# Optimization experiments

Hardware: AMD Instinct MI355X
Metric: run time of the kernel (lower is better)

## Reference

```python
import jax, jax.numpy as jnp
import numpy as np

B, N, C, H = 32, 384, 768, 12
EPS = 1e-6

def setup_inputs() -> dict:
    key = jax.random.key(0)
    k0, k1, k2, k3 = jax.random.split(key, 4)
    x = jax.random.normal(k0, (B, N, C), dtype=jnp.float32)
    # binary keep-mask over key tokens, broadcastable to [B,1,N,N]
    policy = (jax.random.uniform(k1, (B, 1, 1, N)) > 0.5).astype(jnp.float32)
    qkv_w = jax.random.normal(k2, (3 * C, C), dtype=jnp.float32) * 0.02
    qkv_b = jnp.zeros((3 * C,), dtype=jnp.float32)
    proj_w = jax.random.normal(k3, (C, C), dtype=jnp.float32) * 0.02
    proj_b = jnp.zeros((C,), dtype=jnp.float32)
    return {"x": x, "policy": policy, "qkv_w": qkv_w, "qkv_b": qkv_b,
            "proj_w": proj_w, "proj_b": proj_b}

def reference(x, policy, qkv_w, qkv_b, proj_w, proj_b):
    b, n, c = x.shape
    hd = c // H
    scale = hd ** -0.5
    qkv = (x @ qkv_w.T + qkv_b).reshape(b, n, 3, H, hd).transpose(2, 0, 3, 1, 4)
    q, k, v = qkv[0], qkv[1], qkv[2]
    attn = jnp.einsum('bhnd,bhmd->bhnm', q, k) * scale  # [B,H,N,N]
    # softmax_with_policy: eye-blend so every token attends to itself,
    # then eps-regularized masked softmax
    eye = jnp.eye(n, dtype=policy.dtype)[None, None]  # [1,1,N,N]
    attn_policy = policy + (1.0 - policy) * eye       # broadcast -> [B,1,N,N]
    max_att = attn.max(axis=-1, keepdims=True)
    e = jnp.exp(attn - max_att) * attn_policy
    attn = (e + EPS / n) / (e.sum(axis=-1, keepdims=True) + EPS)
    out = jnp.einsum('bhnm,bhmd->bnhd', attn, v).reshape(b, n, c)
    return out @ proj_w.T + proj_b
```

## Files before the change

### kernel.cpp

```cpp
#include <hip/hip_runtime.h>

#define BB 32
#define NN 384
#define CC 768
#define HH 12
#define HD 64

typedef __attribute__((ext_vector_type(4))) float f32x4;
typedef __attribute__((ext_vector_type(8))) __bf16 bf16x8;
typedef __attribute__((ext_vector_type(4))) __bf16 bf16x4;

static __device__ __forceinline__ f32x4 mfma16(bf16x8 a, bf16x8 b, f32x4 c) {
    return __builtin_amdgcn_mfma_f32_16x16x32_bf16(a, b, c, 0, 0, 0);
}

static __device__ __forceinline__ void gload_lds16(const void* g, void* l) {
    __builtin_amdgcn_global_load_lds((const __attribute__((address_space(1))) void*)g,
                                     (__attribute__((address_space(3))) void*)l, 16, 0, 0);
}

#define XU   1179648
#define QU   73728
#define QKVU 221184
#define PU   73728
__global__ void cvt_kernel(const float* __restrict__ x, const float* __restrict__ qkv_w,
                           const float* __restrict__ proj_w, __bf16* __restrict__ dst) {
    const int i = blockIdx.x * blockDim.x + threadIdx.x;
    if (i >= XU + QKVU + PU) return;
    const float* src;
    float sc = 1.f;
    if (i < XU) src = x + (size_t)i * 8;
    else if (i < XU + QKVU) {
        src = qkv_w + (size_t)(i - XU) * 8;
        if (i < XU + QU) sc = 0.125f;
    } else src = proj_w + (size_t)(i - XU - QKVU) * 8;
    f32x4 a = *(const f32x4*)src;
    f32x4 b = *(const f32x4*)(src + 4);
    bf16x8 o;
#pragma unroll
    for (int j = 0; j < 4; ++j) { o[j] = (__bf16)(a[j] * sc); o[j + 4] = (__bf16)(b[j] * sc); }
    *(bf16x8*)(dst + (size_t)i * 8) = o;
}

template <int EPI>
__global__ __launch_bounds__(256, 2) void gemm_kernel(
    const __bf16* __restrict__ A, const __bf16* __restrict__ Bw,
    const float* __restrict__ bias,
    __bf16* __restrict__ qkbuf, __bf16* __restrict__ vtbuf,
    float* __restrict__ fout) {
    __shared__ __bf16 SA[2][128 * 64];
    __shared__ __bf16 SB[2][128 * 64];

    const int tid = threadIdx.x;
    const int l = tid & 63;
    const int w = tid >> 6;
    const int g = l >> 4, q16 = l & 15;
    const int mb = blockIdx.x * 128;
    const int nb = blockIdx.y * 128;
    const int wrb = (w >> 1) * 64;
    const int wcb = (w & 1) * 64;
    const int swz = q16 & 7;

    auto stage = [&](int buf, int kt) {
#pragma unroll
        for (int j = 0; j < 4; ++j) {
            const int ci = j * 256 + w * 64 + l;
            const int row = ci >> 3, c = ci & 7;
            const size_t go = (size_t)row * CC + kt * 64 + ((c ^ (row & 7)) << 3);
            gload_lds16(&A[(size_t)mb * CC + go], &SA[buf][(j * 256 + w * 64) * 8]);
            gload_lds16(&Bw[(size_t)nb * CC + go], &SB[buf][(j * 256 + w * 64) * 8]);
        }
    };

    f32x4 acc[4][4] = {};

    stage(0, 0);
    __syncthreads();

    for (int kt = 0; kt < 12; ++kt) {
        const int buf = kt & 1;
        if (kt < 11) stage(buf ^ 1, kt + 1);
        const char* pa = (const char*)&SA[buf][0];
        const char* pb = (const char*)&SB[buf][0];
#pragma unroll
        for (int c4 = 0; c4 < 2; ++c4) {
            bf16x8 af[4], bfr[4];
#pragma unroll
            for (int m = 0; m < 4; ++m)
                af[m] = *(const bf16x8*)(pa + (wrb + m * 16 + q16) * 128 +
                                         (((c4 * 4 + g) ^ swz) << 4));
#pragma unroll
            for (int n = 0; n < 4; ++n)
                bfr[n] = *(const bf16x8*)(pb + (wcb + n * 16 + q16) * 128 +
                                          (((c4 * 4 + g) ^ swz) << 4));
            __builtin_amdgcn_s_setprio(1);
#pragma unroll
            for (int m = 0; m < 4; ++m)
#pragma unroll
                for (int n = 0; n < 4; ++n)
                    acc[m][n] = mfma16(af[m], bfr[n], acc[m][n]);
            __builtin_amdgcn_s_setprio(0);
        }
        __syncthreads();
    }

    if constexpr (EPI == 0) {
        const int bbatch = mb / NN;
        const int tokb = mb % NN;
#pragma unroll
        for (int n = 0; n < 4; ++n) {
            const int colb = nb + wcb + n * 16;
            const int col = colb + q16;
            float bs = bias[col];
            if (colb < 2 * CC) {
                if (colb < CC) bs *= 0.125f;
#pragma unroll
                for (int m = 0; m < 4; ++m) {
                    const int row = mb + wrb + m * 16 + g * 4;
#pragma unroll
                    for (int r = 0; r < 4; ++r)
                        qkbuf[(size_t)(row + r) * 1536 + col] = (__bf16)(acc[m][n][r] + bs);
                }
            } else {
                const int dd = (col - 2 * CC) & 63;
                const int hh = (colb - 2 * CC) >> 6;
                __bf16* vp = vtbuf + ((size_t)(bbatch * HH + hh) * HD + dd) * NN;
#pragma unroll
                for (int m = 0; m < 4; ++m) {
                    const int tok = tokb + wrb + m * 16 + g * 4;
                    bf16x4 pk;
#pragma unroll
                    for (int r = 0; r < 4; ++r) pk[r] = (__bf16)(acc[m][n][r] + bs);
                    *(bf16x4*)&vp[tok] = pk;
                }
            }
        }
    } else {
#pragma unroll
        for (int n = 0; n < 4; ++n) {
            const int col = nb + wcb + n * 16 + q16;
            const float bs = bias[col];
#pragma unroll
            for (int m = 0; m < 4; ++m)
#pragma unroll
                for (int r = 0; r < 4; ++r)
                    fout[(size_t)(mb + wrb + m * 16 + g * 4 + r) * CC + col] = acc[m][n][r] + bs;
        }
    }
}

__global__ __launch_bounds__(512, 1) void attn_kernel(
    const __bf16* __restrict__ qkbuf, const __bf16* __restrict__ vtbuf,
    const float* __restrict__ policy, __bf16* __restrict__ attb) {
    __shared__ __bf16 Qlds[NN * HD];
    __shared__ __bf16 Klds[NN * HD];
    __shared__ __bf16 Vlds[HD * NN];
    __shared__ float pol[NN];

    const int tid = threadIdx.x;
    const int l = tid & 63;
    const int w = tid >> 6;
    const int g = l >> 4, q16 = l & 15;
    const int bh = blockIdx.x;
    const int b = bh / HH, h = bh % HH;

    const __bf16* qg = qkbuf + (size_t)b * NN * 1536 + h * HD;
    const __bf16* kg = qg + CC;
#pragma unroll
    for (int p = 0; p < 6; ++p) {
        const int cs = p * 512 + w * 64 + l;
        const int row = cs >> 3, cin = cs & 7;
        const size_t go = (size_t)row * 1536 + (size_t)((cin ^ (row & 7)) << 3);
        gload_lds16(&qg[go], &Qlds[(p * 512 + w * 64) * 8]);
        gload_lds16(&kg[go], &Klds[(p * 512 + w * 64) * 8]);
    }
    const __bf16* vg = vtbuf + (size_t)(b * HH + h) * HD * NN;
#pragma unroll
    for (int p = 0; p < 6; ++p) {
        const int cs = p * 512 + w * 64 + l;
        const int row = cs / 48, cin = cs - row * 48;
        gload_lds16(&vg[row * NN + ((cin ^ (row & 7)) << 3)], &Vlds[(p * 512 + w * 64) * 8]);
    }
    for (int i = tid; i < NN; i += 512) pol[i] = policy[b * NN + i];
    __syncthreads();

    const int sw = (q16 & 7) << 4;

    unsigned kw0 = 0, kw1 = 0, kw2 = 0;
#pragma unroll
    for (int kt = 0; kt < 6; ++kt)
#pragma unroll
        for (int t = 0; t < 4; ++t)
#pragma unroll
            for (int r = 0; r < 4; ++r) {
                const int key = kt * 64 + t * 16 + g * 4 + r;
                const unsigned bset = (pol[key] > 0.5f) ? 1u : 0u;
                const int bit = kt * 16 + t * 4 + r;
                if (bit < 32) kw0 |= bset << bit;
                else if (bit < 64) kw1 |= bset << (bit - 32);
                else kw2 |= bset << (bit - 64);
            }

#pragma unroll 1
    for (int ps = 0; ps < 3; ++ps) {
        const int qrow = ps * 128 + w * 16 + q16;
        const int qbyte0 = qrow * 128 + g * 16;
        const bf16x8 qf0 = *(const bf16x8*)((const char*)Qlds + (qbyte0 ^ sw));
        const bf16x8 qf1 = *(const bf16x8*)((const char*)Qlds + ((qbyte0 + 64) ^ sw));

        unsigned pw0 = kw0, pw1 = kw1, pw2 = kw2;
        if (((qrow >> 2) & 3) == g) {
            const int sbit = (qrow >> 6) * 16 + ((qrow >> 4) & 3) * 4 + (qrow & 3);
            if (sbit < 32) pw0 |= 1u << sbit;
            else if (sbit < 64) pw1 |= 1u << (sbit - 32);
            else pw2 |= 1u << (sbit - 64);
        }

        f32x4 oacc[4] = {};
        f32x4 ssum = {0.f, 0.f, 0.f, 0.f};

#pragma unroll 2
        for (int kt = 0; kt < 6; ++kt) {
            f32x4 st[4];
            __builtin_amdgcn_s_setprio(1);
#pragma unroll
            for (int t = 0; t < 4; ++t) {
                const int byte0 = ((kt * 4 + t) * 16 + q16) * 128 + g * 16;
                bf16x8 k0 = *(const bf16x8*)((const char*)Klds + (byte0 ^ sw));
                bf16x8 k1 = *(const bf16x8*)((const char*)Klds + ((byte0 + 64) ^ sw));
                f32x4 z = {0.f, 0.f, 0.f, 0.f};
                st[t] = mfma16(k1, qf1, mfma16(k0, qf0, z));
            }
            __builtin_amdgcn_s_setprio(0);

#pragma unroll
            for (int t = 0; t < 4; ++t) {
#pragma unroll
                for (int r = 0; r < 4; ++r) {
                    const int bit = kt * 16 + t * 4 + r;
                    const unsigned wsel = (bit < 32) ? pw0 : ((bit < 64) ? pw1 : pw2);
                    const bool keep = (wsel >> (bit & 31)) & 1u;
                    st[t][r] = keep ? __expf(st[t][r]) : 0.f;
                }
                ssum += st[t];
            }

            __builtin_amdgcn_s_setprio(1);
#pragma unroll
            for (int c4 = 0; c4 < 2; ++c4) {
                bf16x8 pf;
#pragma unroll
                for (int r = 0; r < 4; ++r) {
                    pf[r] = (__bf16)st[2 * c4][r];
                    pf[r + 4] = (__bf16)st[2 * c4 + 1][r];
                }
                const int c = kt * 2 + c4;
#pragma unroll
                for (int db = 0; db < 4; ++db) {
                    const int byte0 = (db * 16 + q16) * 768 + c * 64 + g * 8;
                    bf16x4 v0 = *(const bf16x4*)((const char*)Vlds + (byte0 ^ sw));
                    bf16x4 v1 = *(const bf16x4*)((const char*)Vlds + ((byte0 + 32) ^ sw));
                    bf16x8 vf;
#pragma unroll
                    for (int r = 0; r < 4; ++r) { vf[r] = v0[r]; vf[r + 4] = v1[r]; }
                    oacc[db] = mfma16(vf, pf, oacc[db]);
                }
            }
            __builtin_amdgcn_s_setprio(0);
        }

        float sum = (ssum[0] + ssum[1]) + (ssum[2] + ssum[3]);
        sum += __shfl_xor(sum, 16);
        sum += __shfl_xor(sum, 32);
        const float dinv = 1.f / (sum + 1e-6f);

        __bf16* op = attb + ((size_t)b * NN + qrow) * CC + h * HD;
#pragma unroll
        for (int db = 0; db < 4; ++db) {
            bf16x4 pk;
#pragma unroll
            for (int r = 0; r < 4; ++r) pk[r] = (__bf16)(oacc[db][r] * dinv);
            *(bf16x4*)&op[db * 16 + g * 4] = pk;
        }
    }
}

extern "C" void kernel_launch(void* const* d_in, const int* in_sizes, int n_in,
                              void* d_out, int out_size, void* d_ws, size_t ws_size,
                              hipStream_t stream) {
    (void)in_sizes; (void)n_in; (void)out_size; (void)ws_size;
    const float* x      = (const float*)d_in[0];
    const float* policy = (const float*)d_in[1];
    const float* qkv_w  = (const float*)d_in[2];
    const float* qkv_b  = (const float*)d_in[3];
    const float* proj_w = (const float*)d_in[4];
    const float* proj_b = (const float*)d_in[5];
    float* out = (float*)d_out;

    __bf16* xb    = (__bf16*)d_ws;
    __bf16* wqkv  = xb + (size_t)12288 * 768;
    __bf16* wproj = wqkv + (size_t)2304 * 768;
    __bf16* qkbuf = wproj + (size_t)768 * 768;
    __bf16* vtbuf = qkbuf + (size_t)12288 * 1536;
    __bf16* attb  = vtbuf + (size_t)BB * HH * HD * NN;

    const int units = XU + QKVU + PU;
    cvt_kernel<<<(units + 255) / 256, 256, 0, stream>>>(x, qkv_w, proj_w, xb);

    gemm_kernel<0><<<dim3(96, 18), 256, 0, stream>>>(xb, wqkv, qkv_b, qkbuf, vtbuf, nullptr);
    attn_kernel<<<384, 512, 0, stream>>>(qkbuf, vtbuf, policy, attb);
    gemm_kernel<1><<<dim3(96, 6), 256, 0, stream>>>(attb, wproj, proj_b, nullptr, nullptr, out);
}
```

Measured before the change: 140.0 us.

## Read Q/K from global in attention, raise occupancy, swizzle GEMM block order

The attention kernel no longer stages Q and K in LDS. Each wave reads its Q and K fragments straight from global memory, leaving only V and the policy in shared memory, and the launch bound is raised so several blocks can be resident per CU. The GEMM kernel remaps its block index so consecutive workgroups are spread across groups of eight, meant to improve L2 locality across chiplets. The trade-off is repeated global/L2 reads of K by every wave in place of one shared LDS copy, plus possible register pressure under the tighter occupancy bound.

```diff
diff --git a/kernel.cpp b/kernel.cpp
--- a/kernel.cpp
+++ b/kernel.cpp
@@ -55,8 +55,13 @@
     const int l = tid & 63;
     const int w = tid >> 6;
     const int g = l >> 4, q16 = l & 15;
-    const int mb = blockIdx.x * 128;
-    const int nb = blockIdx.y * 128;
+
+    const int nwg = gridDim.x * gridDim.y;
+    const int lin = blockIdx.y * gridDim.x + blockIdx.x;
+    const int logical = (lin & 7) * (nwg >> 3) + (lin >> 3);
+    const int mb = (logical % gridDim.x) * 128;
+    const int nb = (logical / gridDim.x) * 128;
+
     const int wrb = (w >> 1) * 64;
     const int wcb = (w & 1) * 64;
     const int swz = q16 & 7;
@@ -149,11 +154,9 @@
     }
 }
 
-__global__ __launch_bounds__(512, 1) void attn_kernel(
+__global__ __launch_bounds__(512, 4) void attn_kernel(
     const __bf16* __restrict__ qkbuf, const __bf16* __restrict__ vtbuf,
     const float* __restrict__ policy, __bf16* __restrict__ attb) {
-    __shared__ __bf16 Qlds[NN * HD];
-    __shared__ __bf16 Klds[NN * HD];
     __shared__ __bf16 Vlds[HD * NN];
     __shared__ float pol[NN];
 
@@ -164,16 +167,6 @@
     const int bh = blockIdx.x;
     const int b = bh / HH, h = bh % HH;
 
-    const __bf16* qg = qkbuf + (size_t)b * NN * 1536 + h * HD;
-    const __bf16* kg = qg + CC;
-#pragma unroll
-    for (int p = 0; p < 6; ++p) {
-        const int cs = p * 512 + w * 64 + l;
-        const int row = cs >> 3, cin = cs & 7;
-        const size_t go = (size_t)row * 1536 + (size_t)((cin ^ (row & 7)) << 3);
-        gload_lds16(&qg[go], &Qlds[(p * 512 + w * 64) * 8]);
-        gload_lds16(&kg[go], &Klds[(p * 512 + w * 64) * 8]);
-    }
     const __bf16* vg = vtbuf + (size_t)(b * HH + h) * HD * NN;
 #pragma unroll
     for (int p = 0; p < 6; ++p) {
@@ -185,6 +178,8 @@
     __syncthreads();
 
     const int sw = (q16 & 7) << 4;
+    const __bf16* qg0 = qkbuf + (size_t)b * NN * 1536 + h * HD;
+    const __bf16* kg = qg0 + CC;
 
     unsigned kw0 = 0, kw1 = 0, kw2 = 0;
 #pragma unroll
@@ -204,9 +199,9 @@
 #pragma unroll 1
     for (int ps = 0; ps < 3; ++ps) {
         const int qrow = ps * 128 + w * 16 + q16;
-        const int qbyte0 = qrow * 128 + g * 16;
-        const bf16x8 qf0 = *(const bf16x8*)((const char*)Qlds + (qbyte0 ^ sw));
-        const bf16x8 qf1 = *(const bf16x8*)((const char*)Qlds + ((qbyte0 + 64) ^ sw));
+        const __bf16* qg = qg0 + (size_t)qrow * 1536;
+        const bf16x8 qf0 = *(const bf16x8*)&qg[g * 8];
+        const bf16x8 qf1 = *(const bf16x8*)&qg[32 + g * 8];
 
         unsigned pw0 = kw0, pw1 = kw1, pw2 = kw2;
         if (((qrow >> 2) & 3) == g) {
@@ -225,9 +220,9 @@
             __builtin_amdgcn_s_setprio(1);
 #pragma unroll
             for (int t = 0; t < 4; ++t) {
-                const int byte0 = ((kt * 4 + t) * 16 + q16) * 128 + g * 16;
-                bf16x8 k0 = *(const bf16x8*)((const char*)Klds + (byte0 ^ sw));
-                bf16x8 k1 = *(const bf16x8*)((const char*)Klds + ((byte0 + 64) ^ sw));
+                const __bf16* kr = &kg[(size_t)((kt * 4 + t) * 16 + q16) * 1536];
+                bf16x8 k0 = *(const bf16x8*)&kr[g * 8];
+                bf16x8 k1 = *(const bf16x8*)&kr[32 + g * 8];
                 f32x4 z = {0.f, 0.f, 0.f, 0.f};
                 st[t] = mfma16(k1, qf1, mfma16(k0, qf0, z));
             }
```

Measured after the change: 192.4 us. 1.37x slower.
